# Kernel optimization log

Measured on AMD Instinct MI355X. Metric: run time of the kernel, lower is better.

Reference implementation:

```python
import jax, jax.numpy as jnp
import numpy as np

THRESHOLD = 0.5
NEG_POS_RATIO = 3
ALPHA = 1.0
B, P, C, O = 128, 8732, 21, 32


def xy_to_cxcy(xy):
    return jnp.concatenate([(xy[..., 2:] + xy[..., :2]) / 2, xy[..., 2:] - xy[..., :2]], axis=-1)


def cxcy_to_xy(cxcy):
    return jnp.concatenate([cxcy[..., :2] - cxcy[..., 2:] / 2, cxcy[..., :2] + cxcy[..., 2:] / 2], axis=-1)


def cxcy_to_gcxgcy(cxcy, priors_cxcy):
    g_cxcy = (cxcy[..., :2] - priors_cxcy[..., :2]) / (priors_cxcy[..., 2:] / 10.0)
    g_wh = jnp.log(cxcy[..., 2:] / priors_cxcy[..., 2:]) * 5.0
    return jnp.concatenate([g_cxcy, g_wh], axis=-1)


def find_jaccard_overlap(set1, set2):
    # set1: [O,4] xy, set2: [P,4] xy -> [O,P]
    lo = jnp.maximum(set1[:, None, :2], set2[None, :, :2])
    hi = jnp.minimum(set1[:, None, 2:], set2[None, :, 2:])
    inter = jnp.prod(jnp.clip(hi - lo, 0.0), axis=-1)
    a1 = jnp.prod(set1[:, 2:] - set1[:, :2], axis=-1)
    a2 = jnp.prod(set2[:, 2:] - set2[:, :2], axis=-1)
    union = a1[:, None] + a2[None, :] - inter
    return inter / union


def setup_inputs() -> dict:
    key = jax.random.key(0)
    k0, k1, k2, k3, k4, k5, k6 = jax.random.split(key, 7)
    predicted_locs = jax.random.normal(k0, (B, P, 4), jnp.float32)
    predicted_scores = jax.random.normal(k1, (B, P, C), jnp.float32)
    centers = jax.random.uniform(k2, (B, O, 2), jnp.float32, 0.2, 0.8)
    sizes = jax.random.uniform(k3, (B, O, 2), jnp.float32, 0.05, 0.3)
    boxes = jnp.concatenate([centers - sizes / 2, centers + sizes / 2], axis=-1)
    labels = jax.random.randint(k4, (B, O), 0, C)
    p_c = jax.random.uniform(k5, (P, 2), jnp.float32, 0.05, 0.95)
    p_wh = jax.random.uniform(k6, (P, 2), jnp.float32, 0.05, 0.5)
    priors_cxcy = jnp.concatenate([p_c, p_wh], axis=-1)
    return {"predicted_locs": predicted_locs, "predicted_scores": predicted_scores,
            "boxes": boxes, "labels": labels, "priors_cxcy": priors_cxcy}


def reference(predicted_locs, predicted_scores, boxes, labels, priors_cxcy):
    priors_xy = cxcy_to_xy(priors_cxcy)

    def match_one(boxes_i, labels_i):
        overlap = find_jaccard_overlap(boxes_i, priors_xy)           # [O,P]
        overlap_for_each_prior = jnp.max(overlap, axis=0)            # [P]
        object_for_each_prior = jnp.argmax(overlap, axis=0)          # [P]
        prior_for_each_object = jnp.argmax(overlap, axis=1)          # [O]
        object_for_each_prior = object_for_each_prior.at[prior_for_each_object].set(jnp.arange(O))
        overlap_for_each_prior = overlap_for_each_prior.at[prior_for_each_object].set(1.0)
        label_for_each_prior = labels_i[object_for_each_prior]
        label_for_each_prior = jnp.where(overlap_for_each_prior < THRESHOLD, 0, label_for_each_prior)
        true_locs_i = cxcy_to_gcxgcy(xy_to_cxcy(boxes_i[object_for_each_prior]), priors_cxcy)
        return label_for_each_prior, true_locs_i

    true_classes, true_locs = jax.vmap(match_one)(boxes, labels)     # [B,P], [B,P,4]

    positive = true_classes != 0                                     # [B,P]
    n_positives = jnp.sum(positive, axis=1)                          # [B]
    n_pos_total = jnp.sum(n_positives)

    # L1Loss (mean over selected positive elements, 4 per prior)
    abs_diff = jnp.abs(predicted_locs - true_locs)                   # [B,P,4]
    loc_loss = jnp.sum(abs_diff * positive[..., None]) / (n_pos_total.astype(jnp.float32) * 4.0)

    # per-element cross-entropy
    log_p = jax.nn.log_softmax(predicted_scores, axis=-1)            # [B,P,C]
    conf_loss_all = -jnp.take_along_axis(log_p, true_classes[..., None], axis=-1)[..., 0]  # [B,P]

    conf_loss_pos_sum = jnp.sum(jnp.where(positive, conf_loss_all, 0.0))
    conf_loss_neg = jnp.where(positive, 0.0, conf_loss_all)
    conf_loss_neg_sorted = -jnp.sort(-conf_loss_neg, axis=1)         # descending
    n_hard = NEG_POS_RATIO * n_positives                             # [B]
    hard_mask = jnp.arange(P)[None, :] < n_hard[:, None]             # [B,P]
    conf_loss_hard_neg_sum = jnp.sum(jnp.where(hard_mask, conf_loss_neg_sorted, 0.0))

    conf_loss = (conf_loss_hard_neg_sum + conf_loss_pos_sum) / n_pos_total.astype(jnp.float32)
    return conf_loss + ALPHA * loc_loss
```

## Files before the change

### kernel.cpp

```cpp
#include <hip/hip_runtime.h>

#define NB 128
#define NP 8732
#define NO 32
#define NC 21
#define NCHUNK 35


__device__ __forceinline__ float wave64_fmax_u(float m) {
    int v;
    v = __builtin_amdgcn_update_dpp(__float_as_int(m), __float_as_int(m), 0x111, 0xf, 0xf, false);
    m = fmaxf(m, __int_as_float(v));
    v = __builtin_amdgcn_update_dpp(__float_as_int(m), __float_as_int(m), 0x112, 0xf, 0xf, false);
    m = fmaxf(m, __int_as_float(v));
    v = __builtin_amdgcn_update_dpp(__float_as_int(m), __float_as_int(m), 0x114, 0xf, 0xf, false);
    m = fmaxf(m, __int_as_float(v));
    v = __builtin_amdgcn_update_dpp(__float_as_int(m), __float_as_int(m), 0x118, 0xf, 0xf, false);
    m = fmaxf(m, __int_as_float(v));
    v = __builtin_amdgcn_update_dpp(__float_as_int(m), __float_as_int(m), 0x142, 0xf, 0xf, false);
    m = fmaxf(m, __int_as_float(v));
    v = __builtin_amdgcn_update_dpp(__float_as_int(m), __float_as_int(m), 0x143, 0xf, 0xf, false);
    m = fmaxf(m, __int_as_float(v));
    return __int_as_float(__builtin_amdgcn_readlane(__float_as_int(m), 63));
}

__device__ __forceinline__ int wave64_imin_u(int m) {
    int v;
    v = __builtin_amdgcn_update_dpp(m, m, 0x111, 0xf, 0xf, false); m = v < m ? v : m;
    v = __builtin_amdgcn_update_dpp(m, m, 0x112, 0xf, 0xf, false); m = v < m ? v : m;
    v = __builtin_amdgcn_update_dpp(m, m, 0x114, 0xf, 0xf, false); m = v < m ? v : m;
    v = __builtin_amdgcn_update_dpp(m, m, 0x118, 0xf, 0xf, false); m = v < m ? v : m;
    v = __builtin_amdgcn_update_dpp(m, m, 0x142, 0xf, 0xf, false); m = v < m ? v : m;
    v = __builtin_amdgcn_update_dpp(m, m, 0x143, 0xf, 0xf, false); m = v < m ? v : m;
    return __builtin_amdgcn_readlane(m, 63);
}

__global__ __launch_bounds__(256) void k_obj(const float* __restrict__ boxes,
                                             const float* __restrict__ priors,
                                             int* __restrict__ pfor) {
    __shared__ float4 spr[1024];
    int b = blockIdx.y;
    int tid = threadIdx.x, lane = tid & 63, wid = tid >> 6;
    int o0 = blockIdx.x * 8 + wid * 2;

    float4 bx0 = ((const float4*)boxes)[b * NO + o0];
    float4 bx1 = ((const float4*)boxes)[b * NO + o0 + 1];
    float a10 = (bx0.z - bx0.x) * (bx0.w - bx0.y);
    float a11 = (bx1.z - bx1.x) * (bx1.w - bx1.y);

    float bv0 = -1.0f, bv1 = -1.0f;
    int   bp0 = 0,     bp1 = 0;

    for (int c0 = 0; c0 < NP; c0 += 1024) {
        int n = NP - c0; if (n > 1024) n = 1024;
        __syncthreads();
        for (int i = tid; i < n; i += 256)
            spr[i] = ((const float4*)priors)[c0 + i];
        __syncthreads();
#pragma unroll 4
        for (int i = lane; i < n; i += 64) {
            float4 pr = spr[i];
            float x1 = pr.x - pr.z * 0.5f, y1 = pr.y - pr.w * 0.5f;
            float x2 = pr.x + pr.z * 0.5f, y2 = pr.y + pr.w * 0.5f;
            float pa = (x2 - x1) * (y2 - y1);
            int p = c0 + i;
            {
                float lx = fmaxf(bx0.x, x1), ly = fmaxf(bx0.y, y1);
                float hx = fminf(bx0.z, x2), hy = fminf(bx0.w, y2);
                float inter = fmaxf(hx - lx, 0.0f) * fmaxf(hy - ly, 0.0f);
                float iou = inter / (a10 + pa - inter);
                if (iou > bv0) { bv0 = iou; bp0 = p; }
            }
            {
                float lx = fmaxf(bx1.x, x1), ly = fmaxf(bx1.y, y1);
                float hx = fminf(bx1.z, x2), hy = fminf(bx1.w, y2);
                float inter = fmaxf(hx - lx, 0.0f) * fmaxf(hy - ly, 0.0f);
                float iou = inter / (a11 + pa - inter);
                if (iou > bv1) { bv1 = iou; bp1 = p; }
            }
        }
    }
    float m0 = wave64_fmax_u(bv0);
    int mp0 = wave64_imin_u((bv0 == m0) ? bp0 : 0x7FFFFFFF);
    float m1 = wave64_fmax_u(bv1);
    int mp1 = wave64_imin_u((bv1 == m1) ? bp1 : 0x7FFFFFFF);
    if (lane == 0) {
        pfor[b * NO + o0]     = mp0;
        pfor[b * NO + o0 + 1] = mp1;
    }
}

__global__ __launch_bounds__(256) void k_loss(const float* __restrict__ plocs,
                                              const float* __restrict__ scores,
                                              const float* __restrict__ boxes,
                                              const int* __restrict__ labels,
                                              const float* __restrict__ priors,
                                              const int* __restrict__ pfor,
                                              float* __restrict__ confneg,
                                              int* __restrict__ pnp,
                                              double* __restrict__ pd0,
                                              double* __restrict__ pd1,
                                              int* __restrict__ donecnt) {
    __shared__ float4 sbox[NO];
    __shared__ float  sa1[NO];
    __shared__ int    slbl[NO];
    __shared__ int    sfp[NO], sfo[NO];
    __shared__ int    snf;
    int b = blockIdx.y;
    int p0 = blockIdx.x * 256;
    int tid = threadIdx.x;

    if (tid < NO) {
        float4 bx = ((const float4*)boxes)[b * NO + tid];
        sbox[tid] = bx;
        sa1[tid]  = (bx.z - bx.x) * (bx.w - bx.y);
        slbl[tid] = labels[b * NO + tid];
    }
    if (tid < 64) {
        int f = -1, inr = 0;
        if (tid < NO) {
            f = pfor[b * NO + tid];
            inr = (f >= p0) && (f < p0 + 256);
        }
        unsigned long long mask = __ballot(inr);
        if (inr) {
            int rank = __popcll(mask & ((1ull << tid) - 1));
            sfp[rank] = f; sfo[rank] = tid;
        }
        if (tid == 0) snf = __popcll(mask);
    }
    __syncthreads();

    int p = p0 + tid;
    float posconf = 0.0f, locpart = 0.0f;
    int isp = 0;

    if (p < NP) {
        float4 pr = ((const float4*)priors)[p];
        float px1 = pr.x - pr.z * 0.5f, py1 = pr.y - pr.w * 0.5f;
        float px2 = pr.x + pr.z * 0.5f, py2 = pr.y + pr.w * 0.5f;
        float pa  = (px2 - px1) * (py2 - py1);

        float bestv = -1.0f; int besto = 0;
#pragma unroll
        for (int o = 0; o < NO; ++o) {
            float4 bx = sbox[o];
            float lx = fmaxf(bx.x, px1), ly = fmaxf(bx.y, py1);
            float hx = fminf(bx.z, px2), hy = fminf(bx.w, py2);
            float inter = fmaxf(hx - lx, 0.0f) * fmaxf(hy - ly, 0.0f);
            float iou = inter / (sa1[o] + pa - inter);
            if (iou > bestv) { bestv = iou; besto = o; }
        }
        int obj = besto;
        int mat = bestv >= 0.5f ? 1 : 0;
        int nf = snf;
        for (int i = 0; i < nf; ++i)
            if (sfp[i] == p) { obj = sfo[i]; mat = 1; }
        int lbl = mat ? slbl[obj] : 0;

        const float* srow = scores + ((size_t)b * NP + p) * NC;
        const float4* r4 = (const float4*)srow;
        float4 q0 = r4[0], q1 = r4[1], q2 = r4[2], q3 = r4[3], q4 = r4[4];
        float s[NC] = {q0.x, q0.y, q0.z, q0.w, q1.x, q1.y, q1.z, q1.w,
                       q2.x, q2.y, q2.z, q2.w, q3.x, q3.y, q3.z, q3.w,
                       q4.x, q4.y, q4.z, q4.w, srow[20]};
        float m = s[0];
#pragma unroll
        for (int c = 1; c < NC; ++c) m = fmaxf(m, s[c]);
        float sum = 0.0f, sl = s[0];
#pragma unroll
        for (int c = 0; c < NC; ++c) {
            sum += __expf(s[c] - m);
            if (c > 0) sl = (lbl == c) ? s[c] : sl;
        }
        float conf = m + __logf(sum) - sl;

        if (lbl != 0) {
            isp = 1;
            posconf = conf;
            float4 bx = sbox[obj];
            float cx = (bx.x + bx.z) * 0.5f, cy = (bx.y + bx.w) * 0.5f;
            float w = bx.z - bx.x, h = bx.w - bx.y;
            float gx = (cx - pr.x) / (pr.z * 0.1f);
            float gy = (cy - pr.y) / (pr.w * 0.1f);
            float gw = __logf(w / pr.z) * 5.0f;
            float gh = __logf(h / pr.w) * 5.0f;
            float4 pl = ((const float4*)plocs)[(size_t)b * NP + p];
            locpart = fabsf(pl.x - gx) + fabsf(pl.y - gy) +
                      fabsf(pl.z - gw) + fabsf(pl.w - gh);
        }
        confneg[(size_t)b * NP + p] = isp ? 0.0f : conf;
    }

    for (int s = 32; s > 0; s >>= 1) {
        posconf += __shfl_xor(posconf, s, 64);
        locpart += __shfl_xor(locpart, s, 64);
        isp     += __shfl_xor(isp, s, 64);
    }
    __shared__ float w0[4], w1[4];
    __shared__ int wc[4];
    int wid = tid >> 6, lane = tid & 63;
    if (lane == 0) { w0[wid] = posconf; w1[wid] = locpart; wc[wid] = isp; }
    __syncthreads();
    if (tid == 0) {
        int pb = b * NCHUNK + blockIdx.x;
        pd0[pb] = (double)(w0[0] + w0[1] + w0[2] + w0[3]);
        pd1[pb] = (double)(w1[0] + w1[1] + w1[2] + w1[3]);
        pnp[pb] = wc[0] + wc[1] + wc[2] + wc[3];
        if (pb == 0) *donecnt = 0;
    }
}

__global__ __launch_bounds__(1024) void k_topk(const float* __restrict__ confneg,
                                               const int* __restrict__ pnp,
                                               const double* __restrict__ pd0,
                                               const double* __restrict__ pd1,
                                               int* __restrict__ snp,
                                               double* __restrict__ sums,
                                               int* __restrict__ donecnt,
                                               float* __restrict__ out) {
    __shared__ int    si2[2][16];
    __shared__ int    siw[16];
    __shared__ double sdd[16];
    __shared__ int    sk;
    int tid = threadIdx.x, b = blockIdx.x;
    int lane = tid & 63, wid = tid >> 6;

    if (wid == 0) {
        int np_ = 0; double d0 = 0.0, d1 = 0.0;
        if (lane < NCHUNK) {
            int pb = b * NCHUNK + lane;
            np_ = pnp[pb]; d0 = pd0[pb]; d1 = pd1[pb];
        }
        for (int s = 32; s > 0; s >>= 1) {
            np_ += __shfl_xor(np_, s, 64);
            d0  += __shfl_xor(d0, s, 64);
            d1  += __shfl_xor(d1, s, 64);
        }
        if (lane == 0) {
            int k = np_ * 3; if (k > NP) k = NP;
            sk = k;
            snp[b] = np_;
            sums[b * 3 + 1] = d0;
            sums[b * 3 + 2] = d1;
        }
    }

    const float* src = confneg + (size_t)b * NP;
    float val[9];
#pragma unroll
    for (int j = 0; j < 9; ++j) {
        int i = tid + j * 1024;
        val[j] = (i < NP) ? src[i] : 0.0f;
    }
    __syncthreads();
    int k = sk;

    double hn = 0.0;
    if (k > 0) {
        unsigned T = 0;
        int par = 0;
        for (int bit = 30; bit >= 0; --bit) {
            unsigned cand = T | (1u << bit);
            int cnt = 0;
#pragma unroll
            for (int j = 0; j < 9; ++j)
                cnt += __popcll(__ballot(__float_as_uint(val[j]) >= cand));
            if (lane == 0) si2[par][wid] = cnt;
            __syncthreads();
            int t = 0;
#pragma unroll
            for (int w = 0; w < 16; ++w) t += si2[par][w];
            par ^= 1;
            if (t >= k) T = cand;
        }

        int cgt = 0;
        double sgt = 0.0;
#pragma unroll
        for (int j = 0; j < 9; ++j) {
            unsigned u = __float_as_uint(val[j]);
            if (u > T) { cgt++; sgt += (double)val[j]; }
        }
        for (int s = 32; s > 0; s >>= 1) {
            cgt += __shfl_xor(cgt, s, 64);
            sgt += __shfl_xor(sgt, s, 64);
        }
        if (lane == 0) { siw[wid] = cgt; sdd[wid] = sgt; }
        __syncthreads();
        if (tid == 0) {
            int cg = 0; double sg = 0.0;
            for (int w = 0; w < 16; ++w) { cg += siw[w]; sg += sdd[w]; }
            hn = sg + (double)(k - cg) * (double)__uint_as_float(T);
        }
    }
    if (tid == 0) sums[b * 3 + 0] = hn;

    __shared__ int samlast;
    if (tid == 0) {
        __threadfence();
        int prev = atomicAdd(donecnt, 1);
        samlast = (prev == NB - 1) ? 1 : 0;
    }
    __syncthreads();
    if (!samlast) return;
    __threadfence();

    double hnn = 0.0, pc = 0.0, lc = 0.0, npd = 0.0;
    if (tid < NB) {
        hnn = atomicAdd(&sums[tid * 3 + 0], 0.0);
        pc  = atomicAdd(&sums[tid * 3 + 1], 0.0);
        lc  = atomicAdd(&sums[tid * 3 + 2], 0.0);
        npd = (double)atomicAdd((int*)&snp[tid], 0);
    }
    for (int s = 32; s > 0; s >>= 1) {
        hnn += __shfl_xor(hnn, s, 64);
        pc  += __shfl_xor(pc, s, 64);
        lc  += __shfl_xor(lc, s, 64);
        npd += __shfl_xor(npd, s, 64);
    }
    __shared__ double sfin[4][2];
    if (lane == 0 && wid < 2) {
        sfin[0][wid] = hnn; sfin[1][wid] = pc; sfin[2][wid] = lc; sfin[3][wid] = npd;
    }
    __syncthreads();
    if (tid == 0) {
        double H  = sfin[0][0] + sfin[0][1];
        double P  = sfin[1][0] + sfin[1][1];
        double L  = sfin[2][0] + sfin[2][1];
        double nt = sfin[3][0] + sfin[3][1];
        out[0] = (float)((H + P) / nt + L / (nt * 4.0));
    }
}

extern "C" void kernel_launch(void* const* d_in, const int* in_sizes, int n_in,
                              void* d_out, int out_size, void* d_ws, size_t ws_size,
                              hipStream_t stream) {
    const float* plocs  = (const float*)d_in[0];
    const float* scores = (const float*)d_in[1];
    const float* boxes  = (const float*)d_in[2];
    const int*   labels = (const int*)d_in[3];
    const float* priors = (const float*)d_in[4];
    float* out = (float*)d_out;

    char* ws = (char*)d_ws;
    int*    pfor    = (int*)ws;
    double* pd0     = (double*)(ws + 16384);
    double* pd1     = (double*)(ws + 52224);
    int*    pnp     = (int*)(ws + 88064);
    int*    snp     = (int*)(ws + 105984);
    double* sums    = (double*)(ws + 106496);
    int*    donecnt = (int*)(ws + 109568);
    float*  confneg = (float*)(ws + 109824);

    hipLaunchKernelGGL(k_obj, dim3(NO / 8, NB), dim3(256), 0, stream,
                       boxes, priors, pfor);
    hipLaunchKernelGGL(k_loss, dim3(NCHUNK, NB), dim3(256), 0, stream,
                       plocs, scores, boxes, labels, priors, pfor,
                       confneg, pnp, pd0, pd1, donecnt);
    hipLaunchKernelGGL(k_topk, dim3(NB), dim3(1024), 0, stream,
                       confneg, pnp, pd0, pd1, snp, sums, donecnt, out);
}
```

Baseline: 225.0 us.

## Restructure prior-matching, prefetch score rows, and use radix-4 top-k threshold search

```diff
diff --git a/kernel.cpp b/kernel.cpp
--- a/kernel.cpp
+++ b/kernel.cpp
@@ -38,55 +38,70 @@
 __global__ __launch_bounds__(256) void k_obj(const float* __restrict__ boxes,
                                              const float* __restrict__ priors,
                                              int* __restrict__ pfor) {
-    __shared__ float4 spr[1024];
+    __shared__ unsigned long long part[4][4];
     int b = blockIdx.y;
     int tid = threadIdx.x, lane = tid & 63, wid = tid >> 6;
-    int o0 = blockIdx.x * 8 + wid * 2;
-
-    float4 bx0 = ((const float4*)boxes)[b * NO + o0];
-    float4 bx1 = ((const float4*)boxes)[b * NO + o0 + 1];
-    float a10 = (bx0.z - bx0.x) * (bx0.w - bx0.y);
-    float a11 = (bx1.z - bx1.x) * (bx1.w - bx1.y);
-
-    float bv0 = -1.0f, bv1 = -1.0f;
-    int   bp0 = 0,     bp1 = 0;
-
-    for (int c0 = 0; c0 < NP; c0 += 1024) {
-        int n = NP - c0; if (n > 1024) n = 1024;
-        __syncthreads();
-        for (int i = tid; i < n; i += 256)
-            spr[i] = ((const float4*)priors)[c0 + i];
-        __syncthreads();
-#pragma unroll 4
-        for (int i = lane; i < n; i += 64) {
-            float4 pr = spr[i];
+    int o0 = blockIdx.x * 4;
+
+    float4 bx[4]; float a1[4];
+#pragma unroll
+    for (int i = 0; i < 4; ++i) {
+        bx[i] = ((const float4*)boxes)[b * NO + o0 + i];
+        a1[i] = (bx[i].z - bx[i].x) * (bx[i].w - bx[i].y);
+    }
+
+    float bv[4] = {-1.0f, -1.0f, -1.0f, -1.0f};
+    int   bp[4] = {0, 0, 0, 0};
+    const float4* pr4 = (const float4*)priors;
+
+    for (int k = 0; k < 34; ++k) {
+        int p = tid + (k << 8);
+        float4 pr = pr4[p];
+        float x1 = pr.x - pr.z * 0.5f, y1 = pr.y - pr.w * 0.5f;
+        float x2 = pr.x + pr.z * 0.5f, y2 = pr.y + pr.w * 0.5f;
+        float pa = (x2 - x1) * (y2 - y1);
+#pragma unroll
+        for (int i = 0; i < 4; ++i) {
+            float lx = fmaxf(bx[i].x, x1), ly = fmaxf(bx[i].y, y1);
+            float hx = fminf(bx[i].z, x2), hy = fminf(bx[i].w, y2);
+            float inter = fmaxf(hx - lx, 0.0f) * fmaxf(hy - ly, 0.0f);
+            float iou = inter / (a1[i] + pa - inter);
+            if (iou > bv[i]) { bv[i] = iou; bp[i] = p; }
+        }
+    }
+    {
+        int p = tid + 8704;
+        if (p < NP) {
+            float4 pr = pr4[p];
             float x1 = pr.x - pr.z * 0.5f, y1 = pr.y - pr.w * 0.5f;
             float x2 = pr.x + pr.z * 0.5f, y2 = pr.y + pr.w * 0.5f;
             float pa = (x2 - x1) * (y2 - y1);
-            int p = c0 + i;
-            {
-                float lx = fmaxf(bx0.x, x1), ly = fmaxf(bx0.y, y1);
-                float hx = fminf(bx0.z, x2), hy = fminf(bx0.w, y2);
+#pragma unroll
+            for (int i = 0; i < 4; ++i) {
+                float lx = fmaxf(bx[i].x, x1), ly = fmaxf(bx[i].y, y1);
+                float hx = fminf(bx[i].z, x2), hy = fminf(bx[i].w, y2);
                 float inter = fmaxf(hx - lx, 0.0f) * fmaxf(hy - ly, 0.0f);
-                float iou = inter / (a10 + pa - inter);
-                if (iou > bv0) { bv0 = iou; bp0 = p; }
+                float iou = inter / (a1[i] + pa - inter);
+                if (iou > bv[i]) { bv[i] = iou; bp[i] = p; }
             }
-            {
-                float lx = fmaxf(bx1.x, x1), ly = fmaxf(bx1.y, y1);
-                float hx = fminf(bx1.z, x2), hy = fminf(bx1.w, y2);
-                float inter = fmaxf(hx - lx, 0.0f) * fmaxf(hy - ly, 0.0f);
-                float iou = inter / (a11 + pa - inter);
-                if (iou > bv1) { bv1 = iou; bp1 = p; }
-            }
-        }
-    }
-    float m0 = wave64_fmax_u(bv0);
-    int mp0 = wave64_imin_u((bv0 == m0) ? bp0 : 0x7FFFFFFF);
-    float m1 = wave64_fmax_u(bv1);
-    int mp1 = wave64_imin_u((bv1 == m1) ? bp1 : 0x7FFFFFFF);
-    if (lane == 0) {
-        pfor[b * NO + o0]     = mp0;
-        pfor[b * NO + o0 + 1] = mp1;
+        }
+    }
+
+#pragma unroll
+    for (int i = 0; i < 4; ++i) {
+        float m = wave64_fmax_u(bv[i]);
+        int mp = wave64_imin_u((bv[i] == m) ? bp[i] : 0x7FFFFFFF);
+        if (lane == 0)
+            part[wid][i] = ((unsigned long long)__float_as_uint(m) << 32) |
+                           (unsigned long long)(0xFFFFFFFFu - (unsigned)mp);
+    }
+    __syncthreads();
+    if (tid < 4) {
+        unsigned long long best = part[0][tid];
+        if (part[1][tid] > best) best = part[1][tid];
+        if (part[2][tid] > best) best = part[2][tid];
+        if (part[3][tid] > best) best = part[3][tid];
+        pfor[b * NO + o0 + tid] = (int)(0xFFFFFFFFu - (unsigned)(best & 0xFFFFFFFFull));
     }
 }
 
@@ -109,11 +124,18 @@
     int b = blockIdx.y;
     int p0 = blockIdx.x * 256;
     int tid = threadIdx.x;
+    int p = p0 + tid;
+    bool valid = p < NP;
+
+    const float* srow = scores + ((size_t)b * NP + (valid ? p : NP - 1)) * NC;
+    const float4* r4 = (const float4*)srow;
+    float4 q0 = r4[0], q1 = r4[1], q2 = r4[2], q3 = r4[3], q4 = r4[4];
+    float s20 = srow[20];
 
     if (tid < NO) {
-        float4 bx = ((const float4*)boxes)[b * NO + tid];
-        sbox[tid] = bx;
-        sa1[tid]  = (bx.z - bx.x) * (bx.w - bx.y);
+        float4 bxx = ((const float4*)boxes)[b * NO + tid];
+        sbox[tid] = bxx;
+        sa1[tid]  = (bxx.z - bxx.x) * (bxx.w - bxx.y);
         slbl[tid] = labels[b * NO + tid];
     }
     if (tid < 64) {
@@ -131,11 +153,10 @@
     }
     __syncthreads();
 
-    int p = p0 + tid;
     float posconf = 0.0f, locpart = 0.0f;
     int isp = 0;
 
-    if (p < NP) {
+    if (valid) {
         float4 pr = ((const float4*)priors)[p];
         float px1 = pr.x - pr.z * 0.5f, py1 = pr.y - pr.w * 0.5f;
         float px2 = pr.x + pr.z * 0.5f, py2 = pr.y + pr.w * 0.5f;
@@ -144,9 +165,9 @@
         float bestv = -1.0f; int besto = 0;
 #pragma unroll
         for (int o = 0; o < NO; ++o) {
-            float4 bx = sbox[o];
-            float lx = fmaxf(bx.x, px1), ly = fmaxf(bx.y, py1);
-            float hx = fminf(bx.z, px2), hy = fminf(bx.w, py2);
+            float4 bxx = sbox[o];
+            float lx = fmaxf(bxx.x, px1), ly = fmaxf(bxx.y, py1);
+            float hx = fminf(bxx.z, px2), hy = fminf(bxx.w, py2);
             float inter = fmaxf(hx - lx, 0.0f) * fmaxf(hy - ly, 0.0f);
             float iou = inter / (sa1[o] + pa - inter);
             if (iou > bestv) { bestv = iou; besto = o; }
@@ -158,29 +179,25 @@
             if (sfp[i] == p) { obj = sfo[i]; mat = 1; }
         int lbl = mat ? slbl[obj] : 0;
 
-        const float* srow = scores + ((size_t)b * NP + p) * NC;
-        const float4* r4 = (const float4*)srow;
-        float4 q0 = r4[0], q1 = r4[1], q2 = r4[2], q3 = r4[3], q4 = r4[4];
+        float sl = srow[lbl];
+
         float s[NC] = {q0.x, q0.y, q0.z, q0.w, q1.x, q1.y, q1.z, q1.w,
                        q2.x, q2.y, q2.z, q2.w, q3.x, q3.y, q3.z, q3.w,
-                       q4.x, q4.y, q4.z, q4.w, srow[20]};
+                       q4.x, q4.y, q4.z, q4.w, s20};
         float m = s[0];
 #pragma unroll
         for (int c = 1; c < NC; ++c) m = fmaxf(m, s[c]);
-        float sum = 0.0f, sl = s[0];
-#pragma unroll
-        for (int c = 0; c < NC; ++c) {
-            sum += __expf(s[c] - m);
-            if (c > 0) sl = (lbl == c) ? s[c] : sl;
-        }
+        float sum = 0.0f;
+#pragma unroll
+        for (int c = 0; c < NC; ++c) sum += __expf(s[c] - m);
         float conf = m + __logf(sum) - sl;
 
         if (lbl != 0) {
             isp = 1;
             posconf = conf;
-            float4 bx = sbox[obj];
-            float cx = (bx.x + bx.z) * 0.5f, cy = (bx.y + bx.w) * 0.5f;
-            float w = bx.z - bx.x, h = bx.w - bx.y;
+            float4 bxx = sbox[obj];
+            float cx = (bxx.x + bxx.z) * 0.5f, cy = (bxx.y + bxx.w) * 0.5f;
+            float w = bxx.z - bxx.x, h = bxx.w - bxx.y;
             float gx = (cx - pr.x) / (pr.z * 0.1f);
             float gy = (cy - pr.y) / (pr.w * 0.1f);
             float gw = __logf(w / pr.z) * 5.0f;
@@ -219,7 +236,7 @@
                                                double* __restrict__ sums,
                                                int* __restrict__ donecnt,
                                                float* __restrict__ out) {
-    __shared__ int    si2[2][16];
+    __shared__ unsigned long long sq[2][16];
     __shared__ int    siw[16];
     __shared__ double sdd[16];
     __shared__ int    sk;
@@ -260,19 +277,44 @@
     if (k > 0) {
         unsigned T = 0;
         int par = 0;
-        for (int bit = 30; bit >= 0; --bit) {
-            unsigned cand = T | (1u << bit);
+        {
+            unsigned cand = 1u << 30;
             int cnt = 0;
 #pragma unroll
             for (int j = 0; j < 9; ++j)
                 cnt += __popcll(__ballot(__float_as_uint(val[j]) >= cand));
-            if (lane == 0) si2[par][wid] = cnt;
+            if (lane == 0) sq[par][wid] = (unsigned long long)cnt;
             __syncthreads();
-            int t = 0;
-#pragma unroll
-            for (int w = 0; w < 16; ++w) t += si2[par][w];
+            unsigned long long t = 0;
+#pragma unroll
+            for (int w = 0; w < 16; ++w) t += sq[par][w];
             par ^= 1;
-            if (t >= k) T = cand;
+            if ((int)t >= k) T = cand;
+        }
+        for (int sh = 28; sh >= 0; sh -= 2) {
+            unsigned c1 = T | (1u << sh), c2 = T | (2u << sh), c3 = T | (3u << sh);
+            int n1 = 0, n2 = 0, n3 = 0;
+#pragma unroll
+            for (int j = 0; j < 9; ++j) {
+                unsigned u = __float_as_uint(val[j]);
+                n1 += __popcll(__ballot(u >= c1));
+                n2 += __popcll(__ballot(u >= c2));
+                n3 += __popcll(__ballot(u >= c3));
+            }
+            if (lane == 0)
+                sq[par][wid] = (unsigned long long)n1 |
+                               ((unsigned long long)n2 << 20) |
+                               ((unsigned long long)n3 << 40);
+            __syncthreads();
+            unsigned long long t = 0;
+#pragma unroll
+            for (int w = 0; w < 16; ++w) t += sq[par][w];
+            par ^= 1;
+            int t1 = (int)(t & 0xFFFFF), t2 = (int)((t >> 20) & 0xFFFFF),
+                t3 = (int)((t >> 40) & 0xFFFFF);
+            if      (t3 >= k) T = c3;
+            else if (t2 >= k) T = c2;
+            else if (t1 >= k) T = c1;
         }
 
         int cgt = 0;
@@ -353,7 +395,7 @@
     int*    donecnt = (int*)(ws + 109568);
     float*  confneg = (float*)(ws + 109824);
 
-    hipLaunchKernelGGL(k_obj, dim3(NO / 8, NB), dim3(256), 0, stream,
+    hipLaunchKernelGGL(k_obj, dim3(NO / 4, NB), dim3(256), 0, stream,
                        boxes, priors, pfor);
     hipLaunchKernelGGL(k_loss, dim3(NCHUNK, NB), dim3(256), 0, stream,
                        plocs, scores, boxes, labels, priors, pfor,
```

New measurement: 220.4 us. 1.02x faster.
